# Kernel tuning notes

Measured on AMD Instinct MI355X. Metric: run time of the kernel, lower is better.

Reference implementation:

```python
import jax, jax.numpy as jnp
import numpy as np

N = 50000
D = 128
E = 600000


def setup_inputs() -> dict:
    key = jax.random.key(0)
    k1, k2, k3, k4, k5, k6 = jax.random.split(key, 6)
    x = jax.random.normal(k1, (N, D), dtype=jnp.float32)
    edge_index = jax.random.randint(k2, (2, E), 0, N, dtype=jnp.int32)
    s = 1.0 / np.sqrt(D)
    W1 = jax.random.uniform(k3, (D, D), dtype=jnp.float32, minval=-s, maxval=s)
    b1 = jax.random.uniform(k4, (D,), dtype=jnp.float32, minval=-s, maxval=s)
    W2 = jax.random.uniform(k5, (D, D), dtype=jnp.float32, minval=-s, maxval=s)
    b2 = jax.random.uniform(k6, (D,), dtype=jnp.float32, minval=-s, maxval=s)
    return {"x": x, "edge_index": edge_index, "W1": W1, "b1": b1, "W2": W2, "b2": b2}


def _gcn_conv(x, src, dst, W, b):
    # PyG GCNConv (default flow source->target): out[dst] += norm * (x @ W)[src] + b
    n = x.shape[0]
    deg = jax.ops.segment_sum(jnp.ones_like(dst, dtype=x.dtype), dst, num_segments=n)
    dinv = jnp.where(deg > 0, jax.lax.rsqrt(deg), 0.0)
    norm = dinv[src] * dinv[dst]          # [E+N]
    h = x @ W                             # [N, D]
    msg = h[src] * norm[:, None]          # [E+N, D] gather + scale
    out = jax.ops.segment_sum(msg, dst, num_segments=n)
    return out + b


def reference(x, edge_index, W1, b1, W2, b2):
    n = x.shape[0]
    loops = jnp.arange(n, dtype=edge_index.dtype)
    src = jnp.concatenate([edge_index[0], loops])  # add self-loops
    dst = jnp.concatenate([edge_index[1], loops])
    h = jax.nn.relu(_gcn_conv(x, src, dst, W1, b1))
    out = jax.nn.relu(_gcn_conv(h, src, dst, W2, b2))
    return out
```

## Files before the change

kernel.cpp:

```cpp
#include <hip/hip_runtime.h>
#include <stdint.h>

typedef __attribute__((ext_vector_type(8))) short bf16x8;
typedef __attribute__((ext_vector_type(4))) float f32x4;

#define CAP 64

__device__ __forceinline__ float bf2f(unsigned int u) {
    union { unsigned int i; float f; } v; v.i = u << 16; return v.f;
}
__device__ __forceinline__ unsigned int f2bf(float f) {
    union { float f; unsigned int i; } v; v.f = f;
    unsigned int b = v.i;
    b += 0x7FFFu + ((b >> 16) & 1u);
    return b >> 16;
}


__global__ void bucket_kernel(const int* __restrict__ src, const int* __restrict__ dst,
                              int* __restrict__ counts, unsigned short* __restrict__ bucket,
                              int E,
                              const float* __restrict__ W1, const float* __restrict__ W2,
                              unsigned short* __restrict__ Wt1, unsigned short* __restrict__ Wt2) {
    int t = blockIdx.x * 256 + threadIdx.x;
    if (t < 32768) {
        const float* W = (t < 16384) ? W1 : W2;
        unsigned short* O = (t < 16384) ? Wt1 : Wt2;
        int i = t & 16383;
        O[i] = (unsigned short)f2bf(W[(i & 127) * 128 + (i >> 7)]);
    }
    if (t < E) {
        int s = src[t], d = dst[t];
        int slot = atomicAdd(&counts[d], 1);
        if (slot < CAP) bucket[(size_t)d * CAP + slot] = (unsigned short)s;
    }
}


__global__ __launch_bounds__(256) void gemm128(const float* __restrict__ A,
                                               const unsigned short* __restrict__ Wt,
                                               const int* __restrict__ counts,
                                               unsigned short* __restrict__ G, int M) {
    int t = threadIdx.x;
    int wave = t >> 6, lane = t & 63;
    int m0 = (blockIdx.x * 4 + wave) * 16;
    int mrow = lane & 15, quad = lane >> 4;

    int arow = m0 + mrow;
    int srow = arow < M ? arow : M - 1;
    const float* Arow = A + (size_t)srow * 128;

    f32x4 acc[8];
#pragma unroll
    for (int nt = 0; nt < 8; ++nt) acc[nt] = (f32x4){0.f, 0.f, 0.f, 0.f};

#pragma unroll
    for (int kb = 0; kb < 4; ++kb) {
        f32x4 lo = *(const f32x4*)(Arow + kb * 32 + quad * 8);
        f32x4 hi = *(const f32x4*)(Arow + kb * 32 + quad * 8 + 4);
        bf16x8 a;
#pragma unroll
        for (int i = 0; i < 4; ++i) { a[i] = (short)f2bf(lo[i]); a[i + 4] = (short)f2bf(hi[i]); }
#pragma unroll
        for (int nt = 0; nt < 8; ++nt) {
            bf16x8 b = *(const bf16x8*)(Wt + (size_t)(nt * 16 + mrow) * 128 + kb * 32 + quad * 8);
            acc[nt] = __builtin_amdgcn_mfma_f32_16x16x32_bf16(a, b, acc[nt], 0, 0, 0);
        }
    }

#pragma unroll
    for (int r = 0; r < 4; ++r) {
        int row = m0 + quad * 4 + r;
        if (row < M) {
            float dr = rsqrtf((float)counts[row] + 1.0f);
#pragma unroll
            for (int nt = 0; nt < 8; ++nt)
                G[(size_t)row * 128 + nt * 16 + mrow] = (unsigned short)f2bf(acc[nt][r] * dr);
        }
    }
}


__global__ __launch_bounds__(256) void fused_agg_gemm(const unsigned short* __restrict__ g,
                                                      const int* __restrict__ counts,
                                                      const unsigned short* __restrict__ bucket,
                                                      const float* __restrict__ bias,
                                                      const unsigned short* __restrict__ Wt,
                                                      unsigned short* __restrict__ G2, int N) {
    __shared__ __align__(16) unsigned short As[16][136];
    int wave = threadIdx.x >> 6, lane = threadIdx.x & 63;
    const unsigned int* g32 = (const unsigned int*)g;
    int nb0 = blockIdx.x * 16 + wave * 4;

    int degs[4]; int svs[4]; unsigned int hvs[4];
#pragma unroll
    for (int i = 0; i < 4; ++i) {
        int n = min(nb0 + i, N - 1);
        degs[i] = counts[n];
        svs[i]  = bucket[(size_t)n * CAP + lane];
        hvs[i]  = g32[(size_t)n * 64 + lane];
    }
    float2 bv = ((const float2*)bias)[lane];

#pragma unroll 1
    for (int i = 0; i < 4; ++i) {
        int m = min(degs[i], CAP);
        float di = rsqrtf((float)degs[i] + 1.0f);
        float a0 = bf2f(hvs[i] & 0xFFFFu);
        float a1 = bf2f(hvs[i] >> 16);
        float c0 = 0.f, c1 = 0.f;
#pragma unroll 1
        for (int j0 = 0; j0 < m; j0 += 16) {
            const unsigned int* rp[16];
            float w[16];
#pragma unroll
            for (int u = 0; u < 16; ++u) {
                int idx = j0 + u;
                int cid = idx < m ? idx : m - 1;
                int s = __builtin_amdgcn_readlane(svs[i], cid);
                rp[u] = g32 + (size_t)s * 64;
                w[u] = idx < m ? 1.f : 0.f;
            }
            unsigned int v[16];
#pragma unroll
            for (int u = 0; u < 16; ++u) v[u] = rp[u][lane];
#pragma unroll
            for (int u = 0; u < 16; ++u) {
                if (u & 1) {
                    c0 = fmaf(w[u], bf2f(v[u] & 0xFFFFu), c0);
                    c1 = fmaf(w[u], bf2f(v[u] >> 16), c1);
                } else {
                    a0 = fmaf(w[u], bf2f(v[u] & 0xFFFFu), a0);
                    a1 = fmaf(w[u], bf2f(v[u] >> 16), a1);
                }
            }
        }
        float o0 = fmaxf((a0 + c0) * di + bv.x, 0.f);
        float o1 = fmaxf((a1 + c1) * di + bv.y, 0.f);
        *(unsigned int*)&As[wave * 4 + i][lane * 2] = f2bf(o0) | (f2bf(o1) << 16);
    }
    __syncthreads();

    int mrow = lane & 15, quad = lane >> 4;
    f32x4 acc[2];
    acc[0] = (f32x4){0.f, 0.f, 0.f, 0.f};
    acc[1] = (f32x4){0.f, 0.f, 0.f, 0.f};
#pragma unroll
    for (int kb = 0; kb < 4; ++kb) {
        bf16x8 a = *(const bf16x8*)(&As[mrow][kb * 32 + quad * 8]);
#pragma unroll
        for (int q = 0; q < 2; ++q) {
            int nt = wave * 2 + q;
            bf16x8 b = *(const bf16x8*)(Wt + (size_t)(nt * 16 + mrow) * 128 + kb * 32 + quad * 8);
            acc[q] = __builtin_amdgcn_mfma_f32_16x16x32_bf16(a, b, acc[q], 0, 0, 0);
        }
    }
#pragma unroll
    for (int r = 0; r < 4; ++r) {
        int row = blockIdx.x * 16 + quad * 4 + r;
        if (row < N) {
            float dr = rsqrtf((float)counts[row] + 1.0f);
#pragma unroll
            for (int q = 0; q < 2; ++q) {
                int nt = wave * 2 + q;
                G2[(size_t)row * 128 + nt * 16 + mrow] = (unsigned short)f2bf(acc[q][r] * dr);
            }
        }
    }
}


__global__ __launch_bounds__(256) void agg_final(const unsigned short* __restrict__ g,
                                                 const int* __restrict__ counts,
                                                 const unsigned short* __restrict__ bucket,
                                                 const float* __restrict__ bias,
                                                 float* __restrict__ out, int N) {
    int lane = threadIdx.x & 63;
    int n = blockIdx.x * 4 + (threadIdx.x >> 6);
    if (n >= N) return;

    const unsigned int* g32 = (const unsigned int*)g;
    int deg = counts[n];
    int m = min(deg, CAP);
    float di = rsqrtf((float)deg + 1.0f);
    int sv = bucket[(size_t)n * CAP + lane];

    unsigned int hv = g32[(size_t)n * 64 + lane];
    float a0 = bf2f(hv & 0xFFFFu);
    float a1 = bf2f(hv >> 16);
    float c0 = 0.f, c1 = 0.f;

#pragma unroll 1
    for (int j0 = 0; j0 < m; j0 += 16) {
        const unsigned int* rp[16];
        float w[16];
#pragma unroll
        for (int u = 0; u < 16; ++u) {
            int idx = j0 + u;
            int cid = idx < m ? idx : m - 1;
            int s = __builtin_amdgcn_readlane(sv, cid);
            rp[u] = g32 + (size_t)s * 64;
            w[u] = idx < m ? 1.f : 0.f;
        }
        unsigned int v[16];
#pragma unroll
        for (int u = 0; u < 16; ++u) v[u] = rp[u][lane];
#pragma unroll
        for (int u = 0; u < 16; ++u) {
            if (u & 1) {
                c0 = fmaf(w[u], bf2f(v[u] & 0xFFFFu), c0);
                c1 = fmaf(w[u], bf2f(v[u] >> 16), c1);
            } else {
                a0 = fmaf(w[u], bf2f(v[u] & 0xFFFFu), a0);
                a1 = fmaf(w[u], bf2f(v[u] >> 16), a1);
            }
        }
    }

    float2 bv = ((const float2*)bias)[lane];
    float o0 = fmaxf((a0 + c0) * di + bv.x, 0.f);
    float o1 = fmaxf((a1 + c1) * di + bv.y, 0.f);
    ((float2*)out)[(size_t)n * 64 + lane] = make_float2(o0, o1);
}


extern "C" void kernel_launch(void* const* d_in, const int* in_sizes, int n_in,
                              void* d_out, int out_size, void* d_ws, size_t ws_size,
                              hipStream_t stream) {
    const float* x  = (const float*)d_in[0];
    const int*   ei = (const int*)d_in[1];
    const float* W1 = (const float*)d_in[2];
    const float* b1 = (const float*)d_in[3];
    const float* W2 = (const float*)d_in[4];
    const float* b2 = (const float*)d_in[5];
    float* out = (float*)d_out;

    int N = in_sizes[0] / 128;
    int E = in_sizes[1] / 2;
    const int* src = ei;
    const int* dst = ei + E;

    char* p = (char*)d_ws;
    auto alloc = [&](size_t bytes) {
        char* r = p; p += (bytes + 255) & ~(size_t)255; return r;
    };
    int*            counts = (int*)           alloc((size_t)N * 4);
    unsigned short* bucket = (unsigned short*)alloc((size_t)N * CAP * 2);
    unsigned short* g1     = (unsigned short*)alloc((size_t)N * 128 * 2);
    unsigned short* g2     = (unsigned short*)alloc((size_t)N * 128 * 2);
    unsigned short* Wt1    = (unsigned short*)alloc(16384 * 2);
    unsigned short* Wt2    = (unsigned short*)alloc(16384 * 2);

    hipMemsetAsync(counts, 0, (size_t)N * 4, stream);
    bucket_kernel<<<(E + 255) / 256, 256, 0, stream>>>(src, dst, counts, bucket, E,
                                                       W1, W2, Wt1, Wt2);

    gemm128<<<(N + 63) / 64, 256, 0, stream>>>(x, Wt1, counts, g1, N);
    fused_agg_gemm<<<(N + 15) / 16, 256, 0, stream>>>(g1, counts, bucket, b1, Wt2, g2, N);
    agg_final<<<(N + 3) / 4, 256, 0, stream>>>(g2, counts, bucket, b2, out, N);
}
```

Measured before the change: 195.0 us.

## Pad neighbor buckets with a zero sentinel row and batch first-chunk gathers

```diff
diff --git a/kernel.cpp b/kernel.cpp
--- a/kernel.cpp
+++ b/kernel.cpp
@@ -40,8 +40,23 @@
 __global__ __launch_bounds__(256) void gemm128(const float* __restrict__ A,
                                                const unsigned short* __restrict__ Wt,
                                                const int* __restrict__ counts,
+                                               unsigned short* __restrict__ bucket,
                                                unsigned short* __restrict__ G, int M) {
     int t = threadIdx.x;
+
+    {
+        int row = blockIdx.x * 64 + (t >> 2);
+        if (row < M) {
+            int deg = min(counts[row], CAP);
+            int pe = (deg + 15) & ~15;
+            if (pe < 16) pe = 16;
+            for (int idx = deg + (t & 3); idx < pe; idx += 4)
+                bucket[(size_t)row * CAP + idx] = (unsigned short)M;
+        }
+    }
+    if (blockIdx.x == 0 && t < 64)
+        ((unsigned int*)G)[(size_t)M * 64 + t] = 0u;
+
     int wave = t >> 6, lane = t & 63;
     int m0 = (blockIdx.x * 4 + wave) * 16;
     int mrow = lane & 15, quad = lane >> 4;
@@ -81,18 +96,24 @@
 }
 
 
-__global__ __launch_bounds__(256) void fused_agg_gemm(const unsigned short* __restrict__ g,
-                                                      const int* __restrict__ counts,
-                                                      const unsigned short* __restrict__ bucket,
-                                                      const float* __restrict__ bias,
-                                                      const unsigned short* __restrict__ Wt,
-                                                      unsigned short* __restrict__ G2, int N) {
-    __shared__ __align__(16) unsigned short As[16][136];
+template <bool FINAL>
+__global__ __launch_bounds__(256) void agg_kernel(const unsigned short* __restrict__ g,
+                                                  const int* __restrict__ counts,
+                                                  const unsigned short* __restrict__ bucket,
+                                                  const float* __restrict__ bias,
+                                                  const unsigned short* __restrict__ Wt,
+                                                  unsigned short* __restrict__ G2,
+                                                  float* __restrict__ outf,
+                                                  int N) {
+    __shared__ __align__(16) unsigned short As[FINAL ? 1 : 16][136];
     int wave = threadIdx.x >> 6, lane = threadIdx.x & 63;
     const unsigned int* g32 = (const unsigned int*)g;
     int nb0 = blockIdx.x * 16 + wave * 4;
 
-    int degs[4]; int svs[4]; unsigned int hvs[4];
+    if (!FINAL && blockIdx.x == 0 && threadIdx.x < 64)
+        ((unsigned int*)G2)[(size_t)N * 64 + threadIdx.x] = 0u;
+
+    int degs[4]; unsigned int svs[4]; unsigned int hvs[4];
 #pragma unroll
     for (int i = 0; i < 4; ++i) {
         int n = min(nb0 + i, N - 1);
@@ -102,43 +123,59 @@
     }
     float2 bv = ((const float2*)bias)[lane];
 
-#pragma unroll 1
+    unsigned int vv[4][16];
+#pragma unroll
     for (int i = 0; i < 4; ++i) {
-        int m = min(degs[i], CAP);
-        float di = rsqrtf((float)degs[i] + 1.0f);
+#pragma unroll
+        for (int u = 0; u < 16; ++u) {
+            int s = __builtin_amdgcn_readlane(svs[i], u);
+            vv[i][u] = *(g32 + (size_t)s * 64 + lane);
+        }
+    }
+
+#pragma unroll
+    for (int i = 0; i < 4; ++i) {
+        int deg = degs[i];
+        int m = min(deg, CAP);
+        int mr = (m + 15) & ~15;
+        if (mr < 16) mr = 16;
+        float di = rsqrtf((float)deg + 1.0f);
         float a0 = bf2f(hvs[i] & 0xFFFFu);
         float a1 = bf2f(hvs[i] >> 16);
         float c0 = 0.f, c1 = 0.f;
+#pragma unroll
+        for (int u = 0; u < 16; ++u) {
+            unsigned int v = vv[i][u];
+            if (u & 1) { c0 += bf2f(v & 0xFFFFu); c1 += bf2f(v >> 16); }
+            else       { a0 += bf2f(v & 0xFFFFu); a1 += bf2f(v >> 16); }
+        }
 #pragma unroll 1
-        for (int j0 = 0; j0 < m; j0 += 16) {
-            const unsigned int* rp[16];
-            float w[16];
+        for (int j0 = 16; j0 < mr; j0 += 16) {
+            unsigned int v2[16];
 #pragma unroll
             for (int u = 0; u < 16; ++u) {
-                int idx = j0 + u;
-                int cid = idx < m ? idx : m - 1;
-                int s = __builtin_amdgcn_readlane(svs[i], cid);
-                rp[u] = g32 + (size_t)s * 64;
-                w[u] = idx < m ? 1.f : 0.f;
+                int s = __builtin_amdgcn_readlane(svs[i], j0 + u);
+                v2[u] = *(g32 + (size_t)s * 64 + lane);
             }
-            unsigned int v[16];
-#pragma unroll
-            for (int u = 0; u < 16; ++u) v[u] = rp[u][lane];
 #pragma unroll
             for (int u = 0; u < 16; ++u) {
-                if (u & 1) {
-                    c0 = fmaf(w[u], bf2f(v[u] & 0xFFFFu), c0);
-                    c1 = fmaf(w[u], bf2f(v[u] >> 16), c1);
-                } else {
-                    a0 = fmaf(w[u], bf2f(v[u] & 0xFFFFu), a0);
-                    a1 = fmaf(w[u], bf2f(v[u] >> 16), a1);
-                }
+                unsigned int v = v2[u];
+                if (u & 1) { c0 += bf2f(v & 0xFFFFu); c1 += bf2f(v >> 16); }
+                else       { a0 += bf2f(v & 0xFFFFu); a1 += bf2f(v >> 16); }
             }
         }
         float o0 = fmaxf((a0 + c0) * di + bv.x, 0.f);
         float o1 = fmaxf((a1 + c1) * di + bv.y, 0.f);
-        *(unsigned int*)&As[wave * 4 + i][lane * 2] = f2bf(o0) | (f2bf(o1) << 16);
-    }
+        if (FINAL) {
+            int n = nb0 + i;
+            if (n < N) ((float2*)outf)[(size_t)n * 64 + lane] = make_float2(o0, o1);
+        } else {
+            *(unsigned int*)&As[wave * 4 + i][lane * 2] = f2bf(o0) | (f2bf(o1) << 16);
+        }
+    }
+
+    if (FINAL) return;
+
     __syncthreads();
 
     int mrow = lane & 15, quad = lane >> 4;
@@ -167,60 +204,6 @@
             }
         }
     }
-}
-
-
-__global__ __launch_bounds__(256) void agg_final(const unsigned short* __restrict__ g,
-                                                 const int* __restrict__ counts,
-                                                 const unsigned short* __restrict__ bucket,
-                                                 const float* __restrict__ bias,
-                                                 float* __restrict__ out, int N) {
-    int lane = threadIdx.x & 63;
-    int n = blockIdx.x * 4 + (threadIdx.x >> 6);
-    if (n >= N) return;
-
-    const unsigned int* g32 = (const unsigned int*)g;
-    int deg = counts[n];
-    int m = min(deg, CAP);
-    float di = rsqrtf((float)deg + 1.0f);
-    int sv = bucket[(size_t)n * CAP + lane];
-
-    unsigned int hv = g32[(size_t)n * 64 + lane];
-    float a0 = bf2f(hv & 0xFFFFu);
-    float a1 = bf2f(hv >> 16);
-    float c0 = 0.f, c1 = 0.f;
-
-#pragma unroll 1
-    for (int j0 = 0; j0 < m; j0 += 16) {
-        const unsigned int* rp[16];
-        float w[16];
-#pragma unroll
-        for (int u = 0; u < 16; ++u) {
-            int idx = j0 + u;
-            int cid = idx < m ? idx : m - 1;
-            int s = __builtin_amdgcn_readlane(sv, cid);
-            rp[u] = g32 + (size_t)s * 64;
-            w[u] = idx < m ? 1.f : 0.f;
-        }
-        unsigned int v[16];
-#pragma unroll
-        for (int u = 0; u < 16; ++u) v[u] = rp[u][lane];
-#pragma unroll
-        for (int u = 0; u < 16; ++u) {
-            if (u & 1) {
-                c0 = fmaf(w[u], bf2f(v[u] & 0xFFFFu), c0);
-                c1 = fmaf(w[u], bf2f(v[u] >> 16), c1);
-            } else {
-                a0 = fmaf(w[u], bf2f(v[u] & 0xFFFFu), a0);
-                a1 = fmaf(w[u], bf2f(v[u] >> 16), a1);
-            }
-        }
-    }
-
-    float2 bv = ((const float2*)bias)[lane];
-    float o0 = fmaxf((a0 + c0) * di + bv.x, 0.f);
-    float o1 = fmaxf((a1 + c1) * di + bv.y, 0.f);
-    ((float2*)out)[(size_t)n * 64 + lane] = make_float2(o0, o1);
 }
 
 
@@ -246,8 +229,8 @@
     };
     int*            counts = (int*)           alloc((size_t)N * 4);
     unsigned short* bucket = (unsigned short*)alloc((size_t)N * CAP * 2);
-    unsigned short* g1     = (unsigned short*)alloc((size_t)N * 128 * 2);
-    unsigned short* g2     = (unsigned short*)alloc((size_t)N * 128 * 2);
+    unsigned short* g1     = (unsigned short*)alloc((size_t)(N + 1) * 128 * 2);
+    unsigned short* g2     = (unsigned short*)alloc((size_t)(N + 1) * 128 * 2);
     unsigned short* Wt1    = (unsigned short*)alloc(16384 * 2);
     unsigned short* Wt2    = (unsigned short*)alloc(16384 * 2);
 
@@ -255,7 +238,7 @@
     bucket_kernel<<<(E + 255) / 256, 256, 0, stream>>>(src, dst, counts, bucket, E,
                                                        W1, W2, Wt1, Wt2);
 
-    gemm128<<<(N + 63) / 64, 256, 0, stream>>>(x, Wt1, counts, g1, N);
-    fused_agg_gemm<<<(N + 15) / 16, 256, 0, stream>>>(g1, counts, bucket, b1, Wt2, g2, N);
-    agg_final<<<(N + 3) / 4, 256, 0, stream>>>(g2, counts, bucket, b2, out, N);
-}
+    gemm128<<<(N + 63) / 64, 256, 0, stream>>>(x, Wt1, counts, bucket, g1, N);
+    agg_kernel<false><<<(N + 15) / 16, 256, 0, stream>>>(g1, counts, bucket, b1, Wt2, g2, nullptr, N);
+    agg_kernel<true ><<<(N + 15) / 16, 256, 0, stream>>>(g2, counts, bucket, b2, nullptr, nullptr, out, N);
+}
```

After: 192.8 us. Within noise of the previous version (-1.1%).
